# Kernel tuning notes

Hardware: AMD Instinct MI355X
Metric: run time of the kernel (lower is better)

Reference implementation:

```python
import jax, jax.numpy as jnp
import numpy as np

K = 5
PAD = (K - 1) // 2
EPS_NORM = 1e-8
MASS_BOUND = 1e-7


def _window_indices(H, W):
    # For each output location (y,x) and each offset (dy,dx) in the kxk window,
    # compute the flat index of (y+dy, x+dx) in prev space and a validity mask.
    ys, xs = jnp.meshgrid(jnp.arange(H), jnp.arange(W), indexing='ij')  # [H,W]
    offs = jnp.arange(-PAD, PAD + 1)
    dy, dx = jnp.meshgrid(offs, offs, indexing='ij')  # [k,k]
    py = ys[:, :, None, None] + dy[None, None]  # [H,W,k,k]
    px = xs[:, :, None, None] + dx[None, None]
    valid = (py >= 0) & (py < H) & (px >= 0) & (px < W)
    ploc = jnp.clip(py, 0, H - 1) * W + jnp.clip(px, 0, W - 1)
    HW, KK = H * W, K * K
    return ploc.reshape(HW, KK), valid.reshape(HW, KK)


def setup_inputs() -> dict:
    key = jax.random.key(0)
    k1, k2, k3 = jax.random.split(key, 3)
    N, D, H, W = 8, 64, 64, 64
    return {
        'cur_feat': jax.random.normal(k1, (N, D, H, W), dtype=jnp.float32),
        'prev_feat': jax.random.normal(k2, (N, D, H, W), dtype=jnp.float32),
        'prev_mem': jax.random.normal(k3, (N, D, H, W), dtype=jnp.float32),
    }


def reference(cur_feat, prev_feat, prev_mem):
    N, D, H, W = prev_mem.shape
    HW = H * W
    cur = cur_feat.reshape(N, -1, HW)   # [N,Dc,HW]
    prev = prev_feat.reshape(N, -1, HW)
    # torch.norm(x, 0) = number of nonzero entries (scalar per batch)
    nc = jnp.sum(cur != 0, axis=(1, 2)).astype(cur.dtype) + EPS_NORM   # [N]
    npv = jnp.sum(prev != 0, axis=(1, 2)).astype(prev.dtype) + EPS_NORM
    # full cost volume: [N, HW(cur loc), HW(prev loc)], negatives clamped to 0
    aff = jnp.einsum('ndp,ndq->npq', cur, prev) / (nc * npv)[:, None, None]
    aff = jnp.maximum(aff, 0.0)

    ploc, valid = _window_indices(H, W)        # [HW,KK]
    loc = jnp.arange(HW)[:, None]              # [HW,1]
    coef = aff[:, loc, ploc] * valid[None].astype(aff.dtype)  # [N,HW,KK]
    mass = jnp.sum(coef, axis=-1)              # [N,HW]
    zero_mass = jnp.abs(mass) < MASS_BOUND
    w = coef / jnp.where(zero_mass, 1.0, mass)[:, :, None]    # [N,HW,KK]

    pm = prev_mem.reshape(N, D, HW)            # [N,D,HW]
    pm_win = pm[:, :, ploc]                    # [N,D,HW,KK]
    val = jnp.einsum('npk,ndpk->ndp', w, pm_win)  # weighted aggregation
    out = jnp.where(zero_mass[:, None, :], pm, val)  # mass==0 -> passthrough
    return out.reshape(N, D, H, W)
```

## Files before the change

### kernel.cpp

```cpp
#include <hip/hip_runtime.h>

#define N_  8
#define D_  64
#define H_  64
#define W_  64
#define HW_ (H_ * W_)
#define KK  25

#define TAGC 0x69000000u
#define TAGP 0x96000000u

__global__ __launch_bounds__(512, 2) void feature_align_fused(
    const float* __restrict__ cur, const float* __restrict__ prev,
    const float* __restrict__ pm, float* __restrict__ out,
    unsigned int* __restrict__ slots)
{
    __shared__ float red[4][KK][128];
    __shared__ unsigned int scnt[8][2];

    const int bid  = blockIdx.x;
    const int bb   = ((bid & 7) << 5) | (bid >> 3);
    const int n    = bb >> 5;
    const int yp   = bb & 31;
    const int y0   = yp * 2;
    const int lane = threadIdx.x & 63;
    const int dg   = __builtin_amdgcn_readfirstlane(threadIdx.x >> 6);
    const int r    = lane >> 5;
    const int xq   = lane & 31;
    const int x0   = xq * 2;
    const int y    = y0 + r;
    const int pix0 = r * 64 + x0;

    int cb[3];
#pragma unroll
    for (int i = 0; i < 3; ++i)
        cb[i] = min(max(x0 - 2 + 2 * i, 0), W_ - 2);
    unsigned voff[5][3];
#pragma unroll
    for (int ky = 0; ky < 5; ++ky) {
        int qy = min(max(y + ky - 2, 0), H_ - 1);
#pragma unroll
        for (int i = 0; i < 3; ++i)
            voff[ky][i] = (unsigned)((qy * W_ + cb[i]) * 4);
    }
    const unsigned curoff = (unsigned)((y * W_ + x0) * 4);

    const size_t nbase = (size_t)n * D_ * HW_;
    const char* curb  = (const char*)(cur  + nbase + (size_t)dg * 8 * HW_);
    const char* prevb = (const char*)(prev + nbase + (size_t)dg * 8 * HW_);
    const char* pmb   = (const char*)(pm   + nbase + (size_t)dg * 8 * HW_);
    char*       outb  = (char*)(out + nbase + (size_t)dg * 8 * HW_);

    float2 pmc[8];
#pragma unroll
    for (int dd = 0; dd < 8; ++dd)
        pmc[dd] = *(const float2*)(pmb + (size_t)dd * HW_ * 4 + curoff);

    float acc0[KK], acc1[KK];
#pragma unroll
    for (int k = 0; k < KK; ++k) { acc0[k] = 0.f; acc1[k] = 0.f; }

    unsigned int cntc = 0, cntp = 0;
#pragma unroll
    for (int dd = 0; dd < 8; ++dd) {
        const char* cch = curb  + (size_t)dd * HW_ * 4;
        const char* pch = prevb + (size_t)dd * HW_ * 4;
        float2 c = *(const float2*)(cch + curoff);
        float2 t[5][3];
#pragma unroll
        for (int ky = 0; ky < 5; ++ky)
#pragma unroll
            for (int i = 0; i < 3; ++i)
                t[ky][i] = *(const float2*)(pch + voff[ky][i]);

        cntc += (unsigned)__popcll(__ballot(c.x != 0.f));
        cntc += (unsigned)__popcll(__ballot(c.y != 0.f));
        cntp += (unsigned)__popcll(__ballot(t[2][1].x != 0.f));
        cntp += (unsigned)__popcll(__ballot(t[2][1].y != 0.f));

#pragma unroll
        for (int ky = 0; ky < 5; ++ky) {
            float v[6] = { t[ky][0].x, t[ky][0].y, t[ky][1].x,
                           t[ky][1].y, t[ky][2].x, t[ky][2].y };
#pragma unroll
            for (int kx = 0; kx < 5; ++kx) {
                acc0[ky * 5 + kx] = fmaf(c.x, v[kx],     acc0[ky * 5 + kx]);
                acc1[ky * 5 + kx] = fmaf(c.y, v[kx + 1], acc1[ky * 5 + kx]);
            }
        }
    }
    if (lane == 0) { scnt[dg][0] = cntc; scnt[dg][1] = cntp; }

    if (dg < 4) {
#pragma unroll
        for (int k = 0; k < KK; ++k)
            *(float2*)&red[dg][k][pix0] = make_float2(acc0[k], acc1[k]);
    }
    __syncthreads();

    if (threadIdx.x == 0) {
        unsigned int tc = 0, tp = 0;
#pragma unroll
        for (int j = 0; j < 8; ++j) { tc += scnt[j][0]; tp += scnt[j][1]; }
        __hip_atomic_store(&slots[n * 32 + yp],       TAGC | tc,
                           __ATOMIC_RELAXED, __HIP_MEMORY_SCOPE_AGENT);
        __hip_atomic_store(&slots[256 + n * 32 + yp], TAGP | tp,
                           __ATOMIC_RELAXED, __HIP_MEMORY_SCOPE_AGENT);
    }
    if (dg >= 4) {
#pragma unroll
        for (int k = 0; k < KK; ++k) {
            float2 t2 = *(float2*)&red[dg - 4][k][pix0];
            t2.x += acc0[k]; t2.y += acc1[k];
            *(float2*)&red[dg - 4][k][pix0] = t2;
        }
    }
    __syncthreads();

    if (threadIdx.x < 128) {
        const int pix = threadIdx.x;
        const int rr  = pix >> 6;
        const int xx  = pix & 63;

        const int      half = lane >> 5;
        const int      sl   = (half << 8) + n * 32 + (lane & 31);
        const unsigned tagw = half ? TAGP : TAGC;
        unsigned int v;
        do {
            v = __hip_atomic_load(&slots[sl], __ATOMIC_RELAXED,
                                  __HIP_MEMORY_SCOPE_AGENT);
        } while ((v & 0xFF000000u) != tagw || (v & 0x00FFFFFFu) > 8192u);
        unsigned int cnt = v & 0x00FFFFFFu;
#pragma unroll
        for (int s = 16; s >= 1; s >>= 1)
            cnt += __shfl_xor(cnt, s);
        const float nc_f = (float)__shfl(cnt, 0);
        const float np_f = (float)__shfl(cnt, 32);
        const float thr = 1e-7f * (nc_f + 1e-8f) * (np_f + 1e-8f);

        float mass = 0.f;
        float cf[KK];
#pragma unroll
        for (int k = 0; k < KK; ++k) {
            float s = red[0][k][pix] + red[1][k][pix]
                    + red[2][k][pix] + red[3][k][pix];
            int ky = k / 5, kx = k % 5;
            int py  = y0 + rr + ky - 2;
            int pxc = xx + kx - 2;
            bool val = (py >= 0) && (py < H_) && (pxc >= 0) && (pxc < W_);
            float c = val ? fmaxf(s, 0.f) : 0.f;
            cf[k] = c;
            mass += c;
        }
        bool  zero = mass < thr;
        float inv  = zero ? 0.f : 1.0f / mass;
#pragma unroll
        for (int k = 0; k < KK; ++k) red[0][k][pix] = cf[k] * inv;
        red[1][0][pix] = zero ? 1.f : 0.f;
    }
    __syncthreads();

    const float zf0 = red[1][0][pix0];
    const float zf1 = red[1][0][pix0 + 1];

    if (zf0 != 0.f && zf1 != 0.f) {
#pragma unroll
        for (int dd = 0; dd < 8; ++dd)
            *(float2*)(outb + (size_t)dd * HW_ * 4 + curoff) = pmc[dd];
    } else {
        float w0[KK], w1[KK];
#pragma unroll
        for (int k = 0; k < KK; ++k) {
            float2 ww = *(float2*)&red[0][k][pix0];
            w0[k] = ww.x; w1[k] = ww.y;
        }
#pragma unroll
        for (int dd = 0; dd < 8; ++dd) {
            const char* pch = pmb + (size_t)dd * HW_ * 4;
            float2 t2[5][3];
#pragma unroll
            for (int ky = 0; ky < 5; ++ky)
#pragma unroll
                for (int i = 0; i < 3; ++i)
                    t2[ky][i] = *(const float2*)(pch + voff[ky][i]);
            float v0 = 0.f, v1 = 0.f;
#pragma unroll
            for (int ky = 0; ky < 5; ++ky) {
                float v[6] = { t2[ky][0].x, t2[ky][0].y, t2[ky][1].x,
                               t2[ky][1].y, t2[ky][2].x, t2[ky][2].y };
#pragma unroll
                for (int kx = 0; kx < 5; ++kx) {
                    v0 = fmaf(w0[ky * 5 + kx], v[kx],     v0);
                    v1 = fmaf(w1[ky * 5 + kx], v[kx + 1], v1);
                }
            }
            float2 o;
            o.x = (zf0 != 0.f) ? pmc[dd].x : v0;
            o.y = (zf1 != 0.f) ? pmc[dd].y : v1;
            *(float2*)(outb + (size_t)dd * HW_ * 4 + curoff) = o;
        }
    }
}

extern "C" void kernel_launch(void* const* d_in, const int* in_sizes, int n_in,
                              void* d_out, int out_size, void* d_ws, size_t ws_size,
                              hipStream_t stream)
{
    const float* cur  = (const float*)d_in[0];
    const float* prev = (const float*)d_in[1];
    const float* pm   = (const float*)d_in[2];
    float*       out  = (float*)d_out;
    unsigned int* slots = (unsigned int*)d_ws;

    feature_align_fused<<<256, 512, 0, stream>>>(cur, prev, pm, out, slots);
}
```

Before: 104.1 us.

## Stage prev-feature halo rows into LDS via global_load_lds before correlation

Copies the six prev_feat rows (all 64 channels) each block needs into a 96KB shared buffer using asynchronous global-to-LDS loads. The correlation loop then reads its 5x3 float2 window from LDS instead of issuing 15 redundant global loads per channel. The cur values are loaded up front and the prev_mem center loads move after the correlation loop, which shortens live ranges. The large LDS allocation (~147KB total with red) may prevent two blocks from sharing a CU, and the strided LDS reads can hit bank conflicts.

Result: faster. 87.60 us (-15.8%).

```diff
diff --git a/kernel.cpp b/kernel.cpp
--- a/kernel.cpp
+++ b/kernel.cpp
@@ -10,11 +10,15 @@
 #define TAGC 0x69000000u
 #define TAGP 0x96000000u
 
+typedef const __attribute__((address_space(1))) void gbl_as_t;
+typedef __attribute__((address_space(3))) void       lds_as_t;
+
 __global__ __launch_bounds__(512, 2) void feature_align_fused(
     const float* __restrict__ cur, const float* __restrict__ prev,
     const float* __restrict__ pm, float* __restrict__ out,
     unsigned int* __restrict__ slots)
 {
+    __shared__ float plds[6][64][64];
     __shared__ float red[4][KK][128];
     __shared__ unsigned int scnt[8][2];
 
@@ -35,26 +39,35 @@
 #pragma unroll
     for (int i = 0; i < 3; ++i)
         cb[i] = min(max(x0 - 2 + 2 * i, 0), W_ - 2);
-    unsigned voff[5][3];
-#pragma unroll
-    for (int ky = 0; ky < 5; ++ky) {
-        int qy = min(max(y + ky - 2, 0), H_ - 1);
-#pragma unroll
-        for (int i = 0; i < 3; ++i)
-            voff[ky][i] = (unsigned)((qy * W_ + cb[i]) * 4);
-    }
     const unsigned curoff = (unsigned)((y * W_ + x0) * 4);
 
     const size_t nbase = (size_t)n * D_ * HW_;
     const char* curb  = (const char*)(cur  + nbase + (size_t)dg * 8 * HW_);
-    const char* prevb = (const char*)(prev + nbase + (size_t)dg * 8 * HW_);
+    const char* prevn = (const char*)(prev + nbase);
     const char* pmb   = (const char*)(pm   + nbase + (size_t)dg * 8 * HW_);
     char*       outb  = (char*)(out + nbase + (size_t)dg * 8 * HW_);
 
-    float2 pmc[8];
+    float2 curc[8];
 #pragma unroll
     for (int dd = 0; dd < 8; ++dd)
-        pmc[dd] = *(const float2*)(pmb + (size_t)dd * HW_ * 4 + curoff);
+        curc[dd] = *(const float2*)(curb + (size_t)dd * HW_ * 4 + curoff);
+
+#pragma unroll
+    for (int i = 0; i < 12; ++i) {
+        const unsigned u     = (unsigned)(i * 8 + dg);
+        const unsigned o     = u * 1024u + (unsigned)lane * 16u;
+        const unsigned j     = o >> 14;
+        const unsigned ch    = (o >> 8) & 63u;
+        const unsigned cbyte = o & 255u;
+        const int      gr    = min(max(y0 - 2 + (int)j, 0), H_ - 1);
+        const char*    src   = prevn + (size_t)ch * (HW_ * 4)
+                             + (unsigned)(gr * (W_ * 4)) + cbyte;
+        __builtin_amdgcn_global_load_lds(
+            (gbl_as_t*)(const void*)src,
+            (lds_as_t*)(void*)((char*)&plds[0][0][0] + u * 1024u),
+            16, 0, 0);
+    }
+    __syncthreads();
 
     float acc0[KK], acc1[KK];
 #pragma unroll
@@ -63,18 +76,18 @@
     unsigned int cntc = 0, cntp = 0;
 #pragma unroll
     for (int dd = 0; dd < 8; ++dd) {
-        const char* cch = curb  + (size_t)dd * HW_ * 4;
-        const char* pch = prevb + (size_t)dd * HW_ * 4;
-        float2 c = *(const float2*)(cch + curoff);
-        float2 t[5][3];
-#pragma unroll
-        for (int ky = 0; ky < 5; ++ky)
-#pragma unroll
-            for (int i = 0; i < 3; ++i)
-                t[ky][i] = *(const float2*)(pch + voff[ky][i]);
-
+        const int ch = dg * 8 + dd;
+        float2 c = curc[dd];
         cntc += (unsigned)__popcll(__ballot(c.x != 0.f));
         cntc += (unsigned)__popcll(__ballot(c.y != 0.f));
+
+        float2 t[5][3];
+#pragma unroll
+        for (int ky = 0; ky < 5; ++ky)
+#pragma unroll
+            for (int i = 0; i < 3; ++i)
+                t[ky][i] = *(const float2*)&plds[r + ky][ch][cb[i]];
+
         cntp += (unsigned)__popcll(__ballot(t[2][1].x != 0.f));
         cntp += (unsigned)__popcll(__ballot(t[2][1].y != 0.f));
 
@@ -89,6 +102,12 @@
             }
         }
     }
+
+    float2 pmc[8];
+#pragma unroll
+    for (int dd = 0; dd < 8; ++dd)
+        pmc[dd] = *(const float2*)(pmb + (size_t)dd * HW_ * 4 + curoff);
+
     if (lane == 0) { scnt[dg][0] = cntc; scnt[dg][1] = cntp; }
 
     if (dg < 4) {
@@ -168,6 +187,14 @@
         for (int dd = 0; dd < 8; ++dd)
             *(float2*)(outb + (size_t)dd * HW_ * 4 + curoff) = pmc[dd];
     } else {
+        unsigned voff[5][3];
+#pragma unroll
+        for (int ky = 0; ky < 5; ++ky) {
+            int qy = min(max(y + ky - 2, 0), H_ - 1);
+#pragma unroll
+            for (int i = 0; i < 3; ++i)
+                voff[ky][i] = (unsigned)((qy * W_ + cb[i]) * 4);
+        }
         float w0[KK], w1[KK];
 #pragma unroll
         for (int k = 0; k < KK; ++k) {
```
